# Performance work log

Hardware: AMD Instinct MI355X
Metric: run time of the kernel (lower is better)

## Reference

```python
import jax, jax.numpy as jnp
import numpy as np

V, D, N, M, H, W, K = 97, 512, 128, 64, 8, 8, 3
HALF = K // 2
DH = D // H
RPL = M + 3 + K   # key(M) + beta + gate + shift(K) + gamma = 70
WPL = RPL + 2 * M # + erase(M) + add(M) = 198
B, T = 32, 128


def _ln(x, g, b):
    mu = x.mean(-1, keepdims=True)
    var = ((x - mu) ** 2).mean(-1, keepdims=True)
    return (x - mu) / jnp.sqrt(var + 1e-5) * g + b


def _addressing(key, beta, gate, shift, gamma, prev_w, memory):
    # key [B,M], beta/gate/gamma [B,1], shift [B,K], prev_w [B,N], memory [B,N,M]
    eps = 1e-12
    kn = key / (jnp.linalg.norm(key, axis=-1, keepdims=True) + eps)
    mn = memory / (jnp.linalg.norm(memory, axis=-1, keepdims=True) + eps)
    cos = jnp.einsum('bnm,bm->bn', mn, kn)
    wc = jax.nn.softmax(jax.nn.softplus(beta) * cos, axis=-1)
    g = jax.nn.sigmoid(gate)
    wg = g * wc + (1.0 - g) * prev_w
    s = jax.nn.softmax(shift, axis=-1)
    shifted = sum(s[:, k:k + 1] * jnp.roll(wg, k - HALF, axis=-1) for k in range(K))
    gp = 1.0 + jax.nn.softplus(gamma)
    wt = (shifted + eps) ** gp
    return wt / (wt.sum(-1, keepdims=True) + eps)


def setup_inputs() -> dict:
    key = jax.random.key(0)
    ks = jax.random.split(key, 16)
    s = 0.05
    return {
        'x': jax.random.randint(ks[0], (B, T), 0, V),
        'emb': jax.random.normal(ks[1], (V, D)) * 0.02,
        'W_in': jax.random.normal(ks[2], (D, D + M)) * s,
        'b_in': jnp.zeros((D,)),
        'W_qkv': jax.random.normal(ks[3], (3 * D, D)) * s,
        'b_qkv': jnp.zeros((3 * D,)),
        'W_o': jax.random.normal(ks[4], (D, D)) * s,
        'b_o': jnp.zeros((D,)),
        'ln1_g': jnp.ones((D,)), 'ln1_b': jnp.zeros((D,)),
        'W_ff1': jax.random.normal(ks[5], (4 * D, D)) * s,
        'b_ff1': jnp.zeros((4 * D,)),
        'W_ff2': jax.random.normal(ks[6], (D, 4 * D)) * s,
        'b_ff2': jnp.zeros((D,)),
        'ln2_g': jnp.ones((D,)), 'ln2_b': jnp.zeros((D,)),
        'W_tok': jax.random.normal(ks[7], (V, D)) * s,
        'b_tok': jnp.zeros((V,)),
        'W_read': jax.random.normal(ks[8], (RPL, D)) * s,
        'b_read': jnp.zeros((RPL,)),
        'W_write': jax.random.normal(ks[9], (WPL, D)) * s,
        'b_write': jnp.zeros((WPL,)),
    }


def _forward(x, emb, W_in, b_in, W_qkv, b_qkv, W_o, b_o, ln1_g, ln1_b,
             W_ff1, b_ff1, W_ff2, b_ff2, ln2_g, ln2_b, W_tok, b_tok,
             W_read, b_read, W_write, b_write):
    Wq, Wk, Wv = W_qkv[:D], W_qkv[D:2 * D], W_qkv[2 * D:]
    bq, bk, bv = b_qkv[:D], b_qkv[D:2 * D], b_qkv[2 * D:]
    scale = 1.0 / np.sqrt(DH)

    def step(carry, x_t):
        memory, rw, ww, cache, t = carry
        tok = emb[x_t]                                   # [B,D]
        r = jnp.einsum('bn,bnm->bm', rw, memory)         # read vector [B,M]
        wide = jnp.concatenate([tok, r], -1)             # [B,D+M]
        xp = wide @ W_in.T + b_in                        # [B,D]
        q = xp[None]                                     # [1,B,D]
        # kv buffer: cache (detached) + current q, truncated to last W
        kbuf = jnp.concatenate([cache, q], 0)[-W:]       # [W,B,D]
        valid = jnp.arange(W) >= W - jnp.minimum(t + 1, W)
        qh = (xp @ Wq.T + bq).reshape(-1, H, DH)         # [B,H,DH]
        kh = (kbuf @ Wk.T + bk).reshape(W, -1, H, DH)    # [W,B,H,DH]
        vh = (kbuf @ Wv.T + bv).reshape(W, -1, H, DH)
        scores = jnp.einsum('bhe,wbhe->bhw', qh, kh) * scale
        scores = jnp.where(valid[None, None, :], scores, -jnp.inf)
        attn = jax.nn.softmax(scores, axis=-1)
        ctx = jnp.einsum('bhw,wbhe->bhe', attn, vh).reshape(-1, D)
        attn_out = ctx @ W_o.T + b_o
        x2 = _ln(xp + attn_out, ln1_g, ln1_b)
        ff = jax.nn.gelu(x2 @ W_ff1.T + b_ff1, approximate=False) @ W_ff2.T + b_ff2
        out = _ln(x2 + ff, ln2_g, ln2_b)
        logits = out @ W_tok.T + b_tok
        # read head addressing (RH=1)
        rp = out @ W_read.T + b_read
        new_rw = _addressing(rp[:, :M], rp[:, M:M + 1], rp[:, M + 1:M + 2],
                             rp[:, M + 2:M + 2 + K], rp[:, M + 2 + K:M + 3 + K],
                             rw, memory)
        # write head addressing + erase/add (WH=1)
        wp = out @ W_write.T + b_write
        new_ww = _addressing(wp[:, :M], wp[:, M:M + 1], wp[:, M + 1:M + 2],
                             wp[:, M + 2:M + 2 + K], wp[:, M + 2 + K:M + 3 + K],
                             ww, memory)
        erase = jax.nn.sigmoid(wp[:, RPL:RPL + M])       # [B,M]
        add = jnp.tanh(wp[:, RPL + M:])                  # [B,M]
        new_mem = memory * (1.0 - new_ww[:, :, None] * erase[:, None, :]) \
                  + new_ww[:, :, None] * add[:, None, :]
        new_cache = jax.lax.stop_gradient(jnp.concatenate([cache, q], 0)[-W:])
        return (new_mem, new_rw, new_ww, new_cache, t + 1), logits

    Bv = x.shape[0]
    mem0 = jnp.zeros((Bv, N, M), jnp.float32)
    w0 = jnp.zeros((Bv, N), jnp.float32).at[:, 0].set(1.0)
    cache0 = jnp.zeros((W, Bv, D), jnp.float32)
    carry0 = (mem0, w0, w0, cache0, jnp.int32(0))
    _, logits = jax.lax.scan(step, carry0, x.T)          # [T,B,V]
    return jnp.transpose(logits, (1, 0, 2))              # [B,T,V]


def reference(x, emb, W_in, b_in, W_qkv, b_qkv, W_o, b_o, ln1_g, ln1_b,
              W_ff1, b_ff1, W_ff2, b_ff2, ln2_g, ln2_b, W_tok, b_tok,
              W_read, b_read, W_write, b_write):
    return _forward(x, emb, W_in, b_in, W_qkv, b_qkv, W_o, b_o, ln1_g, ln1_b,
                    W_ff1, b_ff1, W_ff2, b_ff2, ln2_g, ln2_b, W_tok, b_tok,
                    W_read, b_read, W_write, b_write)
```

## Files before the change

### kernel.cpp

```cpp
#include <hip/hip_runtime.h>
#include <math.h>

static constexpr int Tc = 128, Vc = 97;

static constexpr size_t T_IN  = 0;
static constexpr size_t T_QKV = T_IN  + (size_t)576*512;
static constexpr size_t T_O   = T_QKV + (size_t)512*1536;
static constexpr size_t T_FF1 = T_O   + (size_t)512*512;
static constexpr size_t T_FF2 = T_FF1 + (size_t)512*2048;
static constexpr size_t T_TOK = T_FF2 + (size_t)2048*512;
static constexpr size_t T_RW  = T_TOK + (size_t)512*128;
static constexpr size_t ARENA = T_RW  + (size_t)512*288;
static constexpr size_t TEAM_STRIDE = 5376;
static constexpr size_t A_XP=0, A_CTX=512, A_Y=1024, A_O=1536, A_RWP=2048,
                        A_COS=2368, A_R=2624, A_H=3136;
static constexpr size_t FLG = ARENA + (size_t)32*TEAM_STRIDE;

__device__ __forceinline__ float softplusf_(float x) { return x > 20.f ? x : log1pf(expf(x)); }
__device__ __forceinline__ float sigmoidf_(float x) { return 1.f / (1.f + expf(-x)); }

__device__ __forceinline__ float wsum(float v) {
#pragma unroll
  for (int o = 1; o < 64; o <<= 1) v += __shfl_xor(v, o);
  return v;
}
__device__ __forceinline__ float wmax(float v) {
#pragma unroll
  for (int o = 1; o < 64; o <<= 1) v = fmaxf(v, __shfl_xor(v, o));
  return v;
}

__device__ __forceinline__ void st_llc(float* p, float v) {
  __hip_atomic_store(p, v, __ATOMIC_RELAXED, __HIP_MEMORY_SCOPE_SYSTEM);
}
__device__ __forceinline__ float ld_llc(const float* p) {
  return __hip_atomic_load(p, __ATOMIC_RELAXED, __HIP_MEMORY_SCOPE_SYSTEM);
}
__device__ __forceinline__ void st_flag(int* p, int v) {
  __hip_atomic_store(p, v, __ATOMIC_RELAXED, __HIP_MEMORY_SCOPE_SYSTEM);
}
__device__ __forceinline__ int ld_flag(const int* p) {
  return __hip_atomic_load(p, __ATOMIC_RELAXED, __HIP_MEMORY_SCOPE_SYSTEM);
}

#define PUBF(stage)                                                      \
  do {                                                                   \
    asm volatile("s_waitcnt vmcnt(0)" ::: "memory");                     \
    __syncthreads();                                                     \
    if (tid == 0) st_flag(flg + (stage)*128 + sq*16, t + 1);             \
  } while (0)

#define WAITF(stage, need)                                               \
  do {                                                                   \
    if (tid == 0) {                                                      \
      for (int q2 = 0; q2 < 8; ++q2) {                                   \
        while (ld_flag(flg + (stage)*128 + q2*16) < (need))              \
          __builtin_amdgcn_s_sleep(1);                                   \
      }                                                                  \
    }                                                                    \
    __syncthreads();                                                     \
    asm volatile("" ::: "memory");                                       \
  } while (0)

template <int CH, int SF4>
__device__ __forceinline__ void mv64(const float* __restrict__ wbase,
                                     const float* __restrict__ src,
                                     float* part, int tid) {
  const int cs = tid >> 4, g = tid & 15;
  const float4* __restrict__ w4 =
      reinterpret_cast<const float4*>(wbase + (size_t)cs * CH * (SF4 * 4)) + g;
  const float* __restrict__ v = src + cs * CH;
  float a0 = 0.f, a1 = 0.f, a2 = 0.f, a3 = 0.f;
#pragma unroll 8
  for (int c = 0; c < CH; ++c) {
    float4 w = w4[(size_t)c * SF4];
    float vv = v[c];
    a0 += vv * w.x; a1 += vv * w.y; a2 += vv * w.z; a3 += vv * w.w;
  }
  *reinterpret_cast<float4*>(part + tid * 4) = make_float4(a0, a1, a2, a3);
}

__device__ __forceinline__ void mv256(const float* __restrict__ wbase,
                                      const float* __restrict__ src,
                                      float* part, int tid) {
  const int cs = tid >> 6, g = tid & 63;
  const float4* __restrict__ w4 =
      reinterpret_cast<const float4*>(wbase + (size_t)cs * 64 * 2048) + g;
  const float* __restrict__ v = src + cs * 64;
  float a0 = 0.f, a1 = 0.f, a2 = 0.f, a3 = 0.f;
#pragma unroll 8
  for (int c = 0; c < 64; ++c) {
    float4 w = w4[(size_t)c * 512];
    float vv = v[c];
    a0 += vv * w.x; a1 += vv * w.y; a2 += vv * w.z; a3 += vv * w.w;
  }
  *reinterpret_cast<float4*>(part + tid * 4) = make_float4(a0, a1, a2, a3);
}

__global__ __launch_bounds__(256) void k_init(const float* __restrict__ W_in,
                                              const float* __restrict__ W_qkv,
                                              const float* __restrict__ W_o,
                                              const float* __restrict__ W_ff1,
                                              const float* __restrict__ W_ff2,
                                              const float* __restrict__ W_tok,
                                              const float* __restrict__ W_read,
                                              const float* __restrict__ W_write,
                                              float* __restrict__ ws) {
  const size_t tid = (size_t)blockIdx.x * 256 + threadIdx.x;
  const size_t nth = (size_t)gridDim.x * 256;
  for (size_t i = tid; i < (size_t)576*512; i += nth) {
    size_t c = i >> 9, j = i & 511;
    ws[T_IN + i] = W_in[j * 576 + c];
  }
  for (size_t i = tid; i < (size_t)512*1536; i += nth) {
    size_t c = i / 1536, j = i % 1536;
    ws[T_QKV + i] = W_qkv[j * 512 + c];
  }
  for (size_t i = tid; i < (size_t)512*512; i += nth) {
    size_t e = i >> 9, j = i & 511;
    ws[T_O + i] = W_o[j * 512 + e];
  }
  for (size_t i = tid; i < (size_t)512*2048; i += nth) {
    size_t d = i >> 11, f = i & 2047;
    ws[T_FF1 + i] = W_ff1[f * 512 + d];
  }
  for (size_t i = tid; i < (size_t)2048*512; i += nth) {
    size_t k = i >> 9, j = i & 511;
    ws[T_FF2 + i] = W_ff2[j * 2048 + k];
  }
  for (size_t i = tid; i < (size_t)512*128; i += nth) {
    size_t d = i >> 7, j = i & 127;
    int qq = (int)(j >> 4), i2 = (int)(j & 15);
    int v = qq * 13 + i2;
    ws[T_TOK + i] = (i2 < 13 && v < 97) ? W_tok[(size_t)v * 512 + d] : 0.f;
  }
  for (size_t i = tid; i < (size_t)512*288; i += nth) {
    size_t d = i / 288, j = i % 288;
    int qq = (int)(j / 36), i2 = (int)(j % 36);
    int idx = qq * 34 + i2;
    float val = 0.f;
    if (i2 < 34 && idx < 268)
      val = (idx < 70) ? W_read[(size_t)idx * 512 + d] : W_write[(size_t)(idx - 70) * 512 + d];
    ws[T_RW + i] = val;
  }
  for (size_t i = tid; i < (size_t)32 * TEAM_STRIDE; i += nth) ws[ARENA + i] = 0.f;
  for (size_t i = tid; i < 32768; i += nth) ((int*)(ws + FLG))[i] = 0;
}

__global__ __launch_bounds__(512) void k_main(
    const int* __restrict__ x, const float* __restrict__ emb,
    const float* __restrict__ b_in, const float* __restrict__ b_qkv,
    const float* __restrict__ b_o,
    const float* __restrict__ ln1g, const float* __restrict__ ln1b,
    const float* __restrict__ b_ff1, const float* __restrict__ b_ff2,
    const float* __restrict__ ln2g, const float* __restrict__ ln2b,
    const float* __restrict__ b_tok,
    const float* __restrict__ b_read, const float* __restrict__ b_write,
    float* __restrict__ ws, float* __restrict__ dout) {
  const float* __restrict__ wt = ws;
  const int wg = blockIdx.x, tid = threadIdx.x;
  const int sq = wg & 7, b = wg >> 3;
  const int wv = tid >> 6, ln = tid & 63;
  float* ar = ws + ARENA + (size_t)b * TEAM_STRIDE;
  int* flg = (int*)(ws + FLG) + b * 1024;

  __shared__ float memS[16 * 64];
  __shared__ float kcS[8 * 64], vcS[8 * 64];
  __shared__ float rwvS[128], wwvS[128], wwnS[128];
  __shared__ float rvec[64];
  __shared__ float wideS[576];
  __shared__ float xpS[512];
  __shared__ float qhS[64];
  __shared__ float scoresS[8], awS[8];
  __shared__ float ctxS[512];
  __shared__ float yS[512], x2S[512], oS[512], onS[512];
  __shared__ float hS[2048];
  __shared__ __align__(16) float part[2048];
  __shared__ float rwpS[268];
  __shared__ float cosS[256];
  __shared__ float redA[8], redB[8];

  for (int i = tid; i < 1024; i += 512) memS[i] = 0.f;
  if (tid < 128) { float v0 = (tid == 0) ? 1.f : 0.f; rwvS[tid] = v0; wwvS[tid] = v0; }
  __syncthreads();

  for (int t = 0; t < Tc; ++t) {
    if (t > 0) {
      WAITF(7, t);
      if (tid < 64) {
        float s = 0.f;
#pragma unroll
        for (int q2 = 0; q2 < 8; ++q2) s += ld_llc(ar + A_R + q2 * 64 + tid);
        rvec[tid] = s;
      }
    } else if (tid < 64) rvec[tid] = 0.f;
    __syncthreads();
    const int tok = x[b * Tc + t];
    for (int i = tid; i < 576; i += 512)
      wideS[i] = (i < 512) ? emb[(size_t)tok * 512 + i] : rvec[i - 512];
    __syncthreads();

    mv64<18, 128>(wt + T_IN + 64 * sq, wideS, part, tid);
    __syncthreads();
    if (tid < 64) {
      float s = 0.f;
#pragma unroll
      for (int cs = 0; cs < 32; ++cs) s += part[cs * 64 + tid];
      st_llc(ar + A_XP + 64 * sq + tid, s + b_in[64 * sq + tid]);
    }
    PUBF(0);
    WAITF(0, t + 1);
    xpS[tid] = ld_llc(ar + A_XP + tid);
    __syncthreads();

    const int slot = t & 7;
    for (int p3 = 0; p3 < 3; ++p3) {
      mv64<16, 384>(wt + T_QKV + p3 * 512 + 64 * sq, xpS, part, tid);
      __syncthreads();
      if (tid < 64) {
        float s = 0.f;
#pragma unroll
        for (int cs = 0; cs < 32; ++cs) s += part[cs * 64 + tid];
        s += b_qkv[p3 * 512 + 64 * sq + tid];
        if (p3 == 0) qhS[tid] = s;
        else if (p3 == 1) kcS[slot * 64 + tid] = s;
        else vcS[slot * 64 + tid] = s;
      }
      __syncthreads();
    }
    if (wv < 8) {
      int st = t - 7 + wv;
      float c = 0.f;
      if (st >= 0) c = qhS[ln] * kcS[(st & 7) * 64 + ln];
      c = wsum(c);
      if (ln == 0) scoresS[wv] = (st >= 0) ? c * 0.125f : -INFINITY;
    }
    __syncthreads();
    if (tid == 0) {
      float mx = -INFINITY;
      for (int j = 0; j < 8; ++j) mx = fmaxf(mx, scoresS[j]);
      float e[8], ssum = 0.f;
      for (int j = 0; j < 8; ++j) { e[j] = expf(scoresS[j] - mx); ssum += e[j]; }
      float inv = 1.f / ssum;
      for (int j = 0; j < 8; ++j) awS[j] = e[j] * inv;
    }
    __syncthreads();
    if (tid < 64) {
      float a = 0.f;
#pragma unroll
      for (int j = 0; j < 8; ++j) {
        int st = t - 7 + j;
        if (st >= 0) a += awS[j] * vcS[(st & 7) * 64 + tid];
      }
      st_llc(ar + A_CTX + 64 * sq + tid, a);
    }
    PUBF(1);
    WAITF(1, t + 1);
    ctxS[tid] = ld_llc(ar + A_CTX + tid);
    __syncthreads();

    mv64<16, 128>(wt + T_O + 64 * sq, ctxS, part, tid);
    __syncthreads();
    if (tid < 64) {
      float s = 0.f;
#pragma unroll
      for (int cs = 0; cs < 32; ++cs) s += part[cs * 64 + tid];
      st_llc(ar + A_Y + 64 * sq + tid, s + b_o[64 * sq + tid] + xpS[64 * sq + tid]);
    }
    PUBF(2);
    WAITF(2, t + 1);
    yS[tid] = ld_llc(ar + A_Y + tid);
    __syncthreads();
    {
      float v = yS[tid];
      float a = wsum(v), b2 = wsum(v * v);
      if (ln == 0) { redA[wv] = a; redB[wv] = b2; }
      __syncthreads();
      float sa = 0.f, sb = 0.f;
#pragma unroll
      for (int i2 = 0; i2 < 8; ++i2) { sa += redA[i2]; sb += redB[i2]; }
      float mu = sa * (1.f / 512.f);
      float var = sb * (1.f / 512.f) - mu * mu;
      float rstd = rsqrtf(var + 1e-5f);
      x2S[tid] = (yS[tid] - mu) * rstd * ln1g[tid] + ln1b[tid];
    }
    __syncthreads();

    mv256(wt + T_FF1 + 256 * sq, x2S, part, tid);
    __syncthreads();
    if (tid < 256) {
      float s = 0.f;
#pragma unroll
      for (int cs = 0; cs < 8; ++cs) s += part[cs * 256 + tid];
      s += b_ff1[256 * sq + tid];
      st_llc(ar + A_H + 256 * sq + tid, 0.5f * s * (1.f + erff(s * 0.70710678118654752f)));
    }
    PUBF(3);
    WAITF(3, t + 1);
    for (int i = tid; i < 2048; i += 512) hS[i] = ld_llc(ar + A_H + i);
    __syncthreads();

    mv64<64, 128>(wt + T_FF2 + 64 * sq, hS, part, tid);
    __syncthreads();
    if (tid < 64) {
      float s = 0.f;
#pragma unroll
      for (int cs = 0; cs < 32; ++cs) s += part[cs * 64 + tid];
      st_llc(ar + A_O + 64 * sq + tid, s + b_ff2[64 * sq + tid] + x2S[64 * sq + tid]);
    }
    PUBF(4);
    WAITF(4, t + 1);
    oS[tid] = ld_llc(ar + A_O + tid);
    __syncthreads();
    {
      float v = oS[tid];
      float a = wsum(v), b2 = wsum(v * v);
      if (ln == 0) { redA[wv] = a; redB[wv] = b2; }
      __syncthreads();
      float sa = 0.f, sb = 0.f;
#pragma unroll
      for (int i2 = 0; i2 < 8; ++i2) { sa += redA[i2]; sb += redB[i2]; }
      float mu = sa * (1.f / 512.f);
      float var = sb * (1.f / 512.f) - mu * mu;
      float rstd = rsqrtf(var + 1e-5f);
      onS[tid] = (oS[tid] - mu) * rstd * ln2g[tid] + ln2b[tid];
    }
    __syncthreads();

    if (tid < 288) {
      const int cs = tid / 9, g = tid % 9;
      const float4* __restrict__ w4 =
          reinterpret_cast<const float4*>(wt + T_RW + (size_t)(cs * 16) * 288 + 36 * sq) + g;
      const float* __restrict__ v = onS + cs * 16;
      float a0 = 0.f, a1 = 0.f, a2 = 0.f, a3 = 0.f;
#pragma unroll
      for (int c = 0; c < 16; ++c) {
        float4 w = w4[(size_t)c * 72];
        float vv = v[c];
        a0 += vv * w.x; a1 += vv * w.y; a2 += vv * w.z; a3 += vv * w.w;
      }
      *reinterpret_cast<float4*>(part + cs * 36 + g * 4) = make_float4(a0, a1, a2, a3);
    }
    __syncthreads();
    if (tid < 34) {
      int idx = 34 * sq + tid;
      if (idx < 268) {
        float s = 0.f;
#pragma unroll
        for (int cs = 0; cs < 32; ++cs) s += part[cs * 36 + tid];
        s += (idx < 70) ? b_read[idx] : b_write[idx - 70];
        st_llc(ar + A_RWP + idx, s);
      }
    }
    PUBF(5);
    if (tid < 128) {
      const int cs = tid >> 2, g = tid & 3;
      const float4* __restrict__ w4 =
          reinterpret_cast<const float4*>(wt + T_TOK + (size_t)(cs * 16) * 128 + 16 * sq) + g;
      const float* __restrict__ v = onS + cs * 16;
      float a0 = 0.f, a1 = 0.f, a2 = 0.f, a3 = 0.f;
#pragma unroll
      for (int c = 0; c < 16; ++c) {
        float4 w = w4[(size_t)c * 32];
        float vv = v[c];
        a0 += vv * w.x; a1 += vv * w.y; a2 += vv * w.z; a3 += vv * w.w;
      }
      *reinterpret_cast<float4*>(part + tid * 4) = make_float4(a0, a1, a2, a3);
    }
    __syncthreads();
    if (tid < 13) {
      int v = 13 * sq + tid;
      if (v < Vc) {
        float s = 0.f;
#pragma unroll
        for (int cs = 0; cs < 32; ++cs) s += part[cs * 16 + tid];
        dout[((size_t)b * Tc + t) * Vc + v] = s + b_tok[v];
      }
    }
    WAITF(5, t + 1);
    if (tid < 268) rwpS[tid] = ld_llc(ar + A_RWP + tid);
    __syncthreads();

    {
#pragma unroll
      for (int p = 0; p < 4; ++p) {
        int j = wv + 8 * p;
        int row = j & 15, ksel = j >> 4;
        const float* key = ksel ? (rwpS + 70) : rwpS;
        float m = memS[row * 64 + ln];
        float pp = m * key[ln], qq = m * m;
#pragma unroll
        for (int o = 1; o < 64; o <<= 1) { pp += __shfl_xor(pp, o); qq += __shfl_xor(qq, o); }
        if (ln == 0) st_llc(ar + A_COS + ksel * 128 + 16 * sq + row, pp / (sqrtf(qq) + 1e-12f));
      }
    }
    PUBF(6);
    WAITF(6, t + 1);
    if (tid < 256) cosS[tid] = ld_llc(ar + A_COS + tid);
    __syncthreads();

    if (wv < 2) {
      const float* P = wv ? (rwpS + 70) : rwpS;
      const float* cosb = cosS + wv * 128;
      float* prevw = wv ? wwvS : rwvS;
      float kk = P[ln];
      float kn2 = wsum(kk * kk);
      float kinv = 1.f / (sqrtf(kn2) + 1e-12f);
      float beta = softplusf_(P[64]);
      float g = sigmoidf_(P[65]);
      float sh0 = P[66], sh1 = P[67], sh2 = P[68];
      float m3 = fmaxf(sh0, fmaxf(sh1, sh2));
      float es0 = expf(sh0 - m3), es1 = expf(sh1 - m3), es2 = expf(sh2 - m3);
      float i3 = 1.f / (es0 + es1 + es2);
      es0 *= i3; es1 *= i3; es2 *= i3;
      float gp = 1.f + softplusf_(P[69]);
      float v0 = beta * cosb[ln] * kinv, v1 = beta * cosb[64 + ln] * kinv;
      float mx = wmax(fmaxf(v0, v1));
      float e0 = expf(v0 - mx), e1 = expf(v1 - mx);
      float einv = 1.f / wsum(e0 + e1);
      float w0 = g * e0 * einv + (1.f - g) * prevw[ln];
      float w1 = g * e1 * einv + (1.f - g) * prevw[64 + ln];
      float w0m = __shfl(w0, (ln + 63) & 63), w1m = __shfl(w1, (ln + 63) & 63);
      float w0p = __shfl(w0, (ln + 1) & 63),  w1p = __shfl(w1, (ln + 1) & 63);
      float prev0 = (ln == 0)  ? w1m : w0m;
      float next0 = (ln == 63) ? w1p : w0p;
      float prev1 = (ln == 0)  ? w0m : w1m;
      float next1 = (ln == 63) ? w0p : w1p;
      float t0 = es0 * next0 + es1 * w0 + es2 * prev0;
      float t1 = es0 * next1 + es1 * w1 + es2 * prev1;
      float wt0 = powf(t0 + 1e-12f, gp), wt1 = powf(t1 + 1e-12f, gp);
      float winv = 1.f / (wsum(wt0 + wt1) + 1e-12f);
      w0 = wt0 * winv; w1 = wt1 * winv;
      prevw[ln] = w0; prevw[64 + ln] = w1;
      if (wv) { wwnS[ln] = w0; wwnS[64 + ln] = w1; }
    }
    __syncthreads();
    for (int i = tid; i < 1024; i += 512) {
      int nl = i >> 6, m = i & 63;
      float e = sigmoidf_(rwpS[140 + m]);
      float a = tanhf(rwpS[204 + m]);
      float wn = wwnS[16 * sq + nl];
      memS[i] = memS[i] * (1.f - wn * e) + wn * a;
    }
    __syncthreads();
    if (tid < 64) {
      float s = 0.f;
#pragma unroll
      for (int nl = 0; nl < 16; ++nl) s += rwvS[16 * sq + nl] * memS[nl * 64 + tid];
      st_llc(ar + A_R + 64 * sq + tid, s);
    }
    PUBF(7);
  }
}

extern "C" void kernel_launch(void* const* d_in, const int* in_sizes, int n_in,
                              void* d_out, int out_size, void* d_ws, size_t ws_size,
                              hipStream_t stream) {
  (void)in_sizes; (void)n_in; (void)out_size; (void)ws_size;
  const int* x = (const int*)d_in[0];
  const float* emb = (const float*)d_in[1];
  const float* W_in = (const float*)d_in[2];
  const float* b_in = (const float*)d_in[3];
  const float* W_qkv = (const float*)d_in[4];
  const float* b_qkv = (const float*)d_in[5];
  const float* W_o = (const float*)d_in[6];
  const float* b_o = (const float*)d_in[7];
  const float* ln1g = (const float*)d_in[8];
  const float* ln1b = (const float*)d_in[9];
  const float* W_ff1 = (const float*)d_in[10];
  const float* b_ff1 = (const float*)d_in[11];
  const float* W_ff2 = (const float*)d_in[12];
  const float* b_ff2 = (const float*)d_in[13];
  const float* ln2g = (const float*)d_in[14];
  const float* ln2b = (const float*)d_in[15];
  const float* W_tok = (const float*)d_in[16];
  const float* b_tok = (const float*)d_in[17];
  const float* W_read = (const float*)d_in[18];
  const float* b_read = (const float*)d_in[19];
  const float* W_write = (const float*)d_in[20];
  const float* b_write = (const float*)d_in[21];
  float* ws = (float*)d_ws;
  float* out = (float*)d_out;

  hipLaunchKernelGGL(k_init, dim3(512), dim3(256), 0, stream,
                     W_in, W_qkv, W_o, W_ff1, W_ff2, W_tok, W_read, W_write, ws);
  hipLaunchKernelGGL(k_main, dim3(256), dim3(512), 0, stream,
                     x, emb, b_in, b_qkv, b_o, ln1g, ln1b, b_ff1, b_ff2,
                     ln2g, ln2b, b_tok, b_read, b_write, ws, out);
}
```

Before: 5.883 ms.

## Fold W_in into QKV weights and cut per-step cross-workgroup barriers from eight to three

Precomputes a fused W_qkv·W_in matrix and bias so Q/K/V come straight from the embedding+read vector, removing the xp broadcast barrier. The output projection and FF2 now use split-K over local head/hidden slices, publishing partial sums that every workgroup reduces, which replaces the ctx and hidden broadcasts. Each workgroup keeps a full replicated memory copy, so the read vector, cosine similarities and memory update run locally without exchanges. The cost is extra redundant compute and LDS per workgroup, larger partial-sum traffic, and an extra fuse kernel at launch.

```diff
diff --git a/kernel.cpp b/kernel.cpp
--- a/kernel.cpp
+++ b/kernel.cpp
@@ -3,17 +3,19 @@
 
 static constexpr int Tc = 128, Vc = 97;
 
-static constexpr size_t T_IN  = 0;
-static constexpr size_t T_QKV = T_IN  + (size_t)576*512;
-static constexpr size_t T_O   = T_QKV + (size_t)512*1536;
-static constexpr size_t T_FF1 = T_O   + (size_t)512*512;
+static constexpr size_t T_FQ  = 0;
+static constexpr size_t BF    = T_FQ + (size_t)576*1536;
+static constexpr size_t T_IN  = BF + 1536;
+static constexpr size_t T_O   = T_IN + (size_t)576*512;
+static constexpr size_t T_FF1 = T_O + (size_t)512*512;
 static constexpr size_t T_FF2 = T_FF1 + (size_t)512*2048;
 static constexpr size_t T_TOK = T_FF2 + (size_t)2048*512;
 static constexpr size_t T_RW  = T_TOK + (size_t)512*128;
-static constexpr size_t ARENA = T_RW  + (size_t)512*288;
-static constexpr size_t TEAM_STRIDE = 5376;
-static constexpr size_t A_XP=0, A_CTX=512, A_Y=1024, A_O=1536, A_RWP=2048,
-                        A_COS=2368, A_R=2624, A_H=3136;
+static constexpr size_t ARENA = T_RW + (size_t)512*288;
+static constexpr size_t TEAM_STRIDE = 8704;
+static constexpr size_t A_YP = 0;
+static constexpr size_t A_OP = 4096;
+static constexpr size_t A_RWP = 8192;
 static constexpr size_t FLG = ARENA + (size_t)32*TEAM_STRIDE;
 
 __device__ __forceinline__ float softplusf_(float x) { return x > 20.f ? x : log1pf(expf(x)); }
@@ -52,21 +54,19 @@
 
 #define WAITF(stage, need)                                               \
   do {                                                                   \
-    if (tid == 0) {                                                      \
-      for (int q2 = 0; q2 < 8; ++q2) {                                   \
-        while (ld_flag(flg + (stage)*128 + q2*16) < (need))              \
-          __builtin_amdgcn_s_sleep(1);                                   \
-      }                                                                  \
+    if (tid < 8) {                                                       \
+      while (ld_flag(flg + (stage)*128 + tid*16) < (need))               \
+        __builtin_amdgcn_s_sleep(1);                                     \
     }                                                                    \
     __syncthreads();                                                     \
     asm volatile("" ::: "memory");                                       \
   } while (0)
 
-template <int CH, int SF4>
-__device__ __forceinline__ void mv64(const float* __restrict__ wbase,
-                                     const float* __restrict__ src,
-                                     float* part, int tid) {
-  const int cs = tid >> 4, g = tid & 15;
+template <int NCH, int CH, int NG, int SF4>
+__device__ __forceinline__ void mvp(const float* __restrict__ wbase,
+                                    const float* __restrict__ src,
+                                    float* part, int tid) {
+  const int cs = tid / NG, g = tid % NG;
   const float4* __restrict__ w4 =
       reinterpret_cast<const float4*>(wbase + (size_t)cs * CH * (SF4 * 4)) + g;
   const float* __restrict__ v = src + cs * CH;
@@ -80,23 +80,6 @@
   *reinterpret_cast<float4*>(part + tid * 4) = make_float4(a0, a1, a2, a3);
 }
 
-__device__ __forceinline__ void mv256(const float* __restrict__ wbase,
-                                      const float* __restrict__ src,
-                                      float* part, int tid) {
-  const int cs = tid >> 6, g = tid & 63;
-  const float4* __restrict__ w4 =
-      reinterpret_cast<const float4*>(wbase + (size_t)cs * 64 * 2048) + g;
-  const float* __restrict__ v = src + cs * 64;
-  float a0 = 0.f, a1 = 0.f, a2 = 0.f, a3 = 0.f;
-#pragma unroll 8
-  for (int c = 0; c < 64; ++c) {
-    float4 w = w4[(size_t)c * 512];
-    float vv = v[c];
-    a0 += vv * w.x; a1 += vv * w.y; a2 += vv * w.z; a3 += vv * w.w;
-  }
-  *reinterpret_cast<float4*>(part + tid * 4) = make_float4(a0, a1, a2, a3);
-}
-
 __global__ __launch_bounds__(256) void k_init(const float* __restrict__ W_in,
                                               const float* __restrict__ W_qkv,
                                               const float* __restrict__ W_o,
@@ -105,16 +88,14 @@
                                               const float* __restrict__ W_tok,
                                               const float* __restrict__ W_read,
                                               const float* __restrict__ W_write,
+                                              const float* __restrict__ b_qkv,
+                                              const float* __restrict__ b_in,
                                               float* __restrict__ ws) {
   const size_t tid = (size_t)blockIdx.x * 256 + threadIdx.x;
   const size_t nth = (size_t)gridDim.x * 256;
   for (size_t i = tid; i < (size_t)576*512; i += nth) {
     size_t c = i >> 9, j = i & 511;
     ws[T_IN + i] = W_in[j * 576 + c];
-  }
-  for (size_t i = tid; i < (size_t)512*1536; i += nth) {
-    size_t c = i / 1536, j = i % 1536;
-    ws[T_QKV + i] = W_qkv[j * 512 + c];
   }
   for (size_t i = tid; i < (size_t)512*512; i += nth) {
     size_t e = i >> 9, j = i & 511;
@@ -143,14 +124,48 @@
       val = (idx < 70) ? W_read[(size_t)idx * 512 + d] : W_write[(size_t)(idx - 70) * 512 + d];
     ws[T_RW + i] = val;
   }
+  for (size_t j = tid; j < 1536; j += nth) {
+    float a = b_qkv[j];
+    const float* r = W_qkv + j * 512;
+    for (int d = 0; d < 512; ++d) a += r[d] * b_in[d];
+    ws[BF + j] = a;
+  }
   for (size_t i = tid; i < (size_t)32 * TEAM_STRIDE; i += nth) ws[ARENA + i] = 0.f;
   for (size_t i = tid; i < 32768; i += nth) ((int*)(ws + FLG))[i] = 0;
 }
 
+__global__ __launch_bounds__(256) void k_fuse(const float* __restrict__ W_qkv,
+                                              const float* __restrict__ W_in,
+                                              float* __restrict__ ws) {
+  __shared__ float As[32][64];
+  __shared__ float Bs[32][96];
+  const int cb = blockIdx.x % 9, jb = blockIdx.x / 9;
+  const int c0 = cb * 64, j0 = jb * 96;
+  const int tid = threadIdx.x;
+  float acc[24];
+#pragma unroll
+  for (int u = 0; u < 24; ++u) acc[u] = 0.f;
+  for (int d0 = 0; d0 < 512; d0 += 32) {
+    __syncthreads();
+    for (int i = tid; i < 32 * 64; i += 256) { int dd = i >> 6, cc = i & 63; As[dd][cc] = W_in[(size_t)(d0 + dd) * 576 + c0 + cc]; }
+    for (int i = tid; i < 32 * 96; i += 256) { int jj = i >> 5, dd = i & 31; Bs[dd][jj] = W_qkv[(size_t)(j0 + jj) * 512 + d0 + dd]; }
+    __syncthreads();
+    const int tc = tid & 63, jbase = (tid >> 6) * 24;
+    for (int dd = 0; dd < 32; ++dd) {
+      float a = As[dd][tc];
+#pragma unroll
+      for (int u = 0; u < 24; ++u) acc[u] += a * Bs[dd][jbase + u];
+    }
+  }
+  const int tc = tid & 63, jbase = (tid >> 6) * 24;
+#pragma unroll
+  for (int u = 0; u < 24; ++u)
+    ws[T_FQ + (size_t)(c0 + tc) * 1536 + j0 + jbase + u] = acc[u];
+}
+
 __global__ __launch_bounds__(512) void k_main(
     const int* __restrict__ x, const float* __restrict__ emb,
-    const float* __restrict__ b_in, const float* __restrict__ b_qkv,
-    const float* __restrict__ b_o,
+    const float* __restrict__ b_in, const float* __restrict__ b_o,
     const float* __restrict__ ln1g, const float* __restrict__ ln1b,
     const float* __restrict__ b_ff1, const float* __restrict__ b_ff2,
     const float* __restrict__ ln2g, const float* __restrict__ ln2b,
@@ -164,71 +179,72 @@
   float* ar = ws + ARENA + (size_t)b * TEAM_STRIDE;
   int* flg = (int*)(ws + FLG) + b * 1024;
 
-  __shared__ float memS[16 * 64];
+  __shared__ float memS[128 * 64];
   __shared__ float kcS[8 * 64], vcS[8 * 64];
   __shared__ float rwvS[128], wwvS[128], wwnS[128];
   __shared__ float rvec[64];
   __shared__ float wideS[576];
-  __shared__ float xpS[512];
+  __shared__ float xpSl[64];
   __shared__ float qhS[64];
   __shared__ float scoresS[8], awS[8];
-  __shared__ float ctxS[512];
+  __shared__ float ctxH[64];
   __shared__ float yS[512], x2S[512], oS[512], onS[512];
-  __shared__ float hS[2048];
+  __shared__ float hSl[256];
   __shared__ __align__(16) float part[2048];
-  __shared__ float rwpS[268];
+  __shared__ float rwpS[272];
   __shared__ float cosS[256];
   __shared__ float redA[8], redB[8];
-
-  for (int i = tid; i < 1024; i += 512) memS[i] = 0.f;
+  __shared__ float eS[64], aS[64];
+
+  for (int i = tid; i < 8192; i += 512) memS[i] = 0.f;
   if (tid < 128) { float v0 = (tid == 0) ? 1.f : 0.f; rwvS[tid] = v0; wwvS[tid] = v0; }
   __syncthreads();
 
   for (int t = 0; t < Tc; ++t) {
-    if (t > 0) {
-      WAITF(7, t);
-      if (tid < 64) {
-        float s = 0.f;
-#pragma unroll
-        for (int q2 = 0; q2 < 8; ++q2) s += ld_llc(ar + A_R + q2 * 64 + tid);
-        rvec[tid] = s;
-      }
-    } else if (tid < 64) rvec[tid] = 0.f;
+    {
+      float a = 0.f;
+#pragma unroll
+      for (int k2 = 0; k2 < 16; ++k2) { int n = wv * 16 + k2; a += rwvS[n] * memS[n * 64 + ln]; }
+      part[wv * 64 + ln] = a;
+    }
+    __syncthreads();
+    if (tid < 64) {
+      float s = 0.f;
+#pragma unroll
+      for (int p = 0; p < 8; ++p) s += part[p * 64 + tid];
+      rvec[tid] = s;
+    }
     __syncthreads();
     const int tok = x[b * Tc + t];
     for (int i = tid; i < 576; i += 512)
       wideS[i] = (i < 512) ? emb[(size_t)tok * 512 + i] : rvec[i - 512];
     __syncthreads();
 
-    mv64<18, 128>(wt + T_IN + 64 * sq, wideS, part, tid);
-    __syncthreads();
-    if (tid < 64) {
-      float s = 0.f;
-#pragma unroll
-      for (int cs = 0; cs < 32; ++cs) s += part[cs * 64 + tid];
-      st_llc(ar + A_XP + 64 * sq + tid, s + b_in[64 * sq + tid]);
-    }
-    PUBF(0);
-    WAITF(0, t + 1);
-    xpS[tid] = ld_llc(ar + A_XP + tid);
-    __syncthreads();
-
     const int slot = t & 7;
     for (int p3 = 0; p3 < 3; ++p3) {
-      mv64<16, 384>(wt + T_QKV + p3 * 512 + 64 * sq, xpS, part, tid);
+      mvp<32, 18, 16, 384>(wt + T_FQ + p3 * 512 + 64 * sq, wideS, part, tid);
       __syncthreads();
       if (tid < 64) {
-        float s = 0.f;
+        float s = wt[BF + p3 * 512 + 64 * sq + tid];
 #pragma unroll
         for (int cs = 0; cs < 32; ++cs) s += part[cs * 64 + tid];
-        s += b_qkv[p3 * 512 + 64 * sq + tid];
         if (p3 == 0) qhS[tid] = s;
         else if (p3 == 1) kcS[slot * 64 + tid] = s;
         else vcS[slot * 64 + tid] = s;
       }
       __syncthreads();
     }
-    if (wv < 8) {
+    mvp<32, 18, 16, 128>(wt + T_IN + 64 * sq, wideS, part, tid);
+    __syncthreads();
+    if (tid < 64) {
+      float s = b_in[64 * sq + tid];
+#pragma unroll
+      for (int cs = 0; cs < 32; ++cs) s += part[cs * 64 + tid];
+      xpSl[tid] = s;
+    }
+    __syncthreads();
+
+    {
       int st = t - 7 + wv;
       float c = 0.f;
       if (st >= 0) c = qhS[ln] * kcS[(st & 7) * 64 + ln];
@@ -252,24 +268,27 @@
         int st = t - 7 + j;
         if (st >= 0) a += awS[j] * vcS[(st & 7) * 64 + tid];
       }
-      st_llc(ar + A_CTX + 64 * sq + tid, a);
-    }
-    PUBF(1);
-    WAITF(1, t + 1);
-    ctxS[tid] = ld_llc(ar + A_CTX + tid);
-    __syncthreads();
-
-    mv64<16, 128>(wt + T_O + 64 * sq, ctxS, part, tid);
-    __syncthreads();
-    if (tid < 64) {
+      ctxH[tid] = a;
+    }
+    __syncthreads();
+
+    mvp<4, 16, 128, 128>(wt + T_O + (size_t)64 * sq * 512, ctxH, part, tid);
+    __syncthreads();
+    {
       float s = 0.f;
 #pragma unroll
-      for (int cs = 0; cs < 32; ++cs) s += part[cs * 64 + tid];
-      st_llc(ar + A_Y + 64 * sq + tid, s + b_o[64 * sq + tid] + xpS[64 * sq + tid]);
-    }
-    PUBF(2);
-    WAITF(2, t + 1);
-    yS[tid] = ld_llc(ar + A_Y + tid);
+      for (int cs = 0; cs < 4; ++cs) s += part[cs * 512 + tid];
+      if ((tid >> 6) == sq) s += xpSl[tid & 63];
+      st_llc(ar + A_YP + sq * 512 + tid, s);
+    }
+    PUBF(0);
+    WAITF(0, t + 1);
+    {
+      float s = b_o[tid];
+#pragma unroll
+      for (int q2 = 0; q2 < 8; ++q2) s += ld_llc(ar + A_YP + q2 * 512 + tid);
+      yS[tid] = s;
+    }
     __syncthreads();
     {
       float v = yS[tid];
@@ -286,31 +305,32 @@
     }
     __syncthreads();
 
-    mv256(wt + T_FF1 + 256 * sq, x2S, part, tid);
+    mvp<8, 64, 64, 512>(wt + T_FF1 + 256 * sq, x2S, part, tid);
     __syncthreads();
     if (tid < 256) {
+      float s = b_ff1[256 * sq + tid];
+#pragma unroll
+      for (int cs = 0; cs < 8; ++cs) s += part[cs * 256 + tid];
+      hSl[tid] = 0.5f * s * (1.f + erff(s * 0.70710678118654752f));
+    }
+    __syncthreads();
+
+    mvp<4, 64, 128, 128>(wt + T_FF2 + (size_t)256 * sq * 512, hSl, part, tid);
+    __syncthreads();
+    {
       float s = 0.f;
 #pragma unroll
-      for (int cs = 0; cs < 8; ++cs) s += part[cs * 256 + tid];
-      s += b_ff1[256 * sq + tid];
-      st_llc(ar + A_H + 256 * sq + tid, 0.5f * s * (1.f + erff(s * 0.70710678118654752f)));
-    }
-    PUBF(3);
-    WAITF(3, t + 1);
-    for (int i = tid; i < 2048; i += 512) hS[i] = ld_llc(ar + A_H + i);
-    __syncthreads();
-
-    mv64<64, 128>(wt + T_FF2 + 64 * sq, hS, part, tid);
-    __syncthreads();
-    if (tid < 64) {
-      float s = 0.f;
-#pragma unroll
-      for (int cs = 0; cs < 32; ++cs) s += part[cs * 64 + tid];
-      st_llc(ar + A_O + 64 * sq + tid, s + b_ff2[64 * sq + tid] + x2S[64 * sq + tid]);
-    }
-    PUBF(4);
-    WAITF(4, t + 1);
-    oS[tid] = ld_llc(ar + A_O + tid);
+      for (int cs = 0; cs < 4; ++cs) s += part[cs * 512 + tid];
+      st_llc(ar + A_OP + sq * 512 + tid, s);
+    }
+    PUBF(1);
+    WAITF(1, t + 1);
+    {
+      float s = b_ff2[tid] + x2S[tid];
+#pragma unroll
+      for (int q2 = 0; q2 < 8; ++q2) s += ld_llc(ar + A_OP + q2 * 512 + tid);
+      oS[tid] = s;
+    }
     __syncthreads();
     {
       float v = oS[tid];
@@ -345,14 +365,13 @@
     if (tid < 34) {
       int idx = 34 * sq + tid;
       if (idx < 268) {
-        float s = 0.f;
+        float s = (idx < 70) ? b_read[idx] : b_write[idx - 70];
 #pragma unroll
         for (int cs = 0; cs < 32; ++cs) s += part[cs * 36 + tid];
-        s += (idx < 70) ? b_read[idx] : b_write[idx - 70];
         st_llc(ar + A_RWP + idx, s);
       }
     }
-    PUBF(5);
+    PUBF(2);
     if (tid < 128) {
       const int cs = tid >> 2, g = tid & 3;
       const float4* __restrict__ w4 =
@@ -371,34 +390,27 @@
     if (tid < 13) {
       int v = 13 * sq + tid;
       if (v < Vc) {
-        float s = 0.f;
+        float s = b_tok[v];
 #pragma unroll
         for (int cs = 0; cs < 32; ++cs) s += part[cs * 16 + tid];
-        dout[((size_t)b * Tc + t) * Vc + v] = s + b_tok[v];
-      }
-    }
-    WAITF(5, t + 1);
+        dout[((size_t)b * Tc + t) * Vc + v] = s;
+      }
+    }
+    WAITF(2, t + 1);
     if (tid < 268) rwpS[tid] = ld_llc(ar + A_RWP + tid);
     __syncthreads();
 
-    {
-#pragma unroll
-      for (int p = 0; p < 4; ++p) {
-        int j = wv + 8 * p;
-        int row = j & 15, ksel = j >> 4;
-        const float* key = ksel ? (rwpS + 70) : rwpS;
-        float m = memS[row * 64 + ln];
-        float pp = m * key[ln], qq = m * m;
-#pragma unroll
-        for (int o = 1; o < 64; o <<= 1) { pp += __shfl_xor(pp, o); qq += __shfl_xor(qq, o); }
-        if (ln == 0) st_llc(ar + A_COS + ksel * 128 + 16 * sq + row, pp / (sqrtf(qq) + 1e-12f));
-      }
-    }
-    PUBF(6);
-    WAITF(6, t + 1);
-    if (tid < 256) cosS[tid] = ld_llc(ar + A_COS + tid);
-    __syncthreads();
-
+    for (int p = 0; p < 32; ++p) {
+      int idx = wv * 32 + p;
+      int ksel = idx >> 7, row = idx & 127;
+      const float* key = ksel ? (rwpS + 70) : rwpS;
+      float m = memS[row * 64 + ln];
+      float pp = m * key[ln], qq = m * m;
+#pragma unroll
+      for (int o = 1; o < 64; o <<= 1) { pp += __shfl_xor(pp, o); qq += __shfl_xor(qq, o); }
+      if (ln == 0) cosS[idx] = pp / (sqrtf(qq) + 1e-12f);
+    }
+    __syncthreads();
     if (wv < 2) {
       const float* P = wv ? (rwpS + 70) : rwpS;
       const float* cosb = cosS + wv * 128;
@@ -433,23 +445,17 @@
       w0 = wt0 * winv; w1 = wt1 * winv;
       prevw[ln] = w0; prevw[64 + ln] = w1;
       if (wv) { wwnS[ln] = w0; wwnS[64 + ln] = w1; }
-    }
-    __syncthreads();
-    for (int i = tid; i < 1024; i += 512) {
-      int nl = i >> 6, m = i & 63;
-      float e = sigmoidf_(rwpS[140 + m]);
-      float a = tanhf(rwpS[204 + m]);
-      float wn = wwnS[16 * sq + nl];
-      memS[i] = memS[i] * (1.f - wn * e) + wn * a;
-    }
-    __syncthreads();
-    if (tid < 64) {
-      float s = 0.f;
-#pragma unroll
-      for (int nl = 0; nl < 16; ++nl) s += rwvS[16 * sq + nl] * memS[nl * 64 + tid];
-      st_llc(ar + A_R + 64 * sq + tid, s);
-    }
-    PUBF(7);
+    } else if (wv == 2) {
+      eS[ln] = sigmoidf_(rwpS[140 + ln]);
+      aS[ln] = tanhf(rwpS[204 + ln]);
+    }
+    __syncthreads();
+    for (int i = tid; i < 8192; i += 512) {
+      int n = i >> 6, m = i & 63;
+      float wn = wwnS[n];
+      memS[i] = memS[i] * (1.f - wn * eS[m]) + wn * aS[m];
+    }
+    __syncthreads();
   }
 }
 
@@ -483,8 +489,10 @@
   float* out = (float*)d_out;
 
   hipLaunchKernelGGL(k_init, dim3(512), dim3(256), 0, stream,
-                     W_in, W_qkv, W_o, W_ff1, W_ff2, W_tok, W_read, W_write, ws);
+                     W_in, W_qkv, W_o, W_ff1, W_ff2, W_tok, W_read, W_write,
+                     b_qkv, b_in, ws);
+  hipLaunchKernelGGL(k_fuse, dim3(144), dim3(256), 0, stream, W_qkv, W_in, ws);
   hipLaunchKernelGGL(k_main, dim3(256), dim3(512), 0, stream,
-                     x, emb, b_in, b_qkv, b_o, ln1g, ln1b, b_ff1, b_ff2,
+                     x, emb, b_in, b_o, ln1g, ln1b, b_ff1, b_ff2,
                      ln2g, ln2b, b_tok, b_read, b_write, ws, out);
 }
```

Measured after the change: 6.163 ms. 1.05x slower.
